# Performance work log

Hardware: AMD Instinct MI355X
Metric: run time of the kernel (lower is better)

## Reference

```python
import jax, jax.numpy as jnp
import numpy as np

S, N, L, D, H, V = 64, 128, 10, 300, 150, 50000


def setup_inputs() -> dict:
    key = jax.random.key(0)
    k0, k1, k2, k3 = jax.random.split(key, 4)
    tokens = jax.random.randint(k0, (S, N), 0, V)
    emb_table = jax.random.normal(k1, (V, D), jnp.float32) * 0.02
    W1 = jax.random.normal(k2, (D, H), jnp.float32) * (1.0 / np.sqrt(D))
    b1 = jnp.zeros((H,), jnp.float32)
    W2 = jax.random.normal(k3, (H, 1), jnp.float32) * (1.0 / np.sqrt(H))
    b2 = jnp.zeros((1,), jnp.float32)
    return {"tokens": tokens, "emb_table": emb_table, "W1": W1, "b1": b1, "W2": W2, "b2": b2}


def reference(tokens, emb_table, W1, b1, W2, b2):
    # word embeddings per sentence: [S, N, D]
    emb = emb_table[tokens]
    # FFNN attention score per token: Linear->ReLU->Linear(->1), squeeze -> [S, N]
    scores = (jax.nn.relu(emb @ W1 + b1) @ W2 + b2)[..., 0]

    n = tokens.shape[1]
    k = jnp.arange(L)                      # window position within span
    pos = jnp.arange(n)
    idx = pos[:, None] + k[None, :]        # [N, L] absolute token index of span (i, i+k)
    valid = idx < n                        # span position in-bounds
    idx_c = jnp.minimum(idx, n - 1)

    win_emb = emb[:, idx_c]                # [S, N, L, D]  emb[s, i+k]
    win_sc = scores[:, idx_c]              # [S, N, L]     scores[s, i+k]

    # tri[w, k] = (k <= w): positions belonging to span of width index w
    tri = k[:, None] >= k[None, :]                       # [L, L]
    m = tri[None, None] & valid[None, :, None, :]        # [1, N, L(w), L(k)]
    logits = jnp.where(m, win_sc[:, :, None, :], -jnp.inf)
    probs = jax.nn.softmax(logits, axis=-1)              # [S, N, Lw, Lk]
    head = jnp.einsum('snwk,snkd->snwd', probs, win_emb)  # softmax-weighted sum

    first = jnp.broadcast_to(emb[:, :, None, :], win_emb.shape)  # emb[i]
    last = win_emb                                               # emb[i+w] at k-axis == w
    out = jnp.concatenate([first, last, head], axis=-1)          # [S, N, L, 3D]
    # zero out spans that run past the sentence end
    return out * valid[None, :, :, None].astype(out.dtype)
```

## Files before the change

### kernel.cpp

```cpp
#include <hip/hip_runtime.h>
#include <cstddef>

#define SS 64
#define NN 128
#define LL 10
#define DD 300
#define HH 150
#define HP 152
#define CC 16
#define RMAX (CC + LL - 1)
#define JG 19
#define TG 13

#define WS_W1P 0
#define WS_BW  (DD*HP)

typedef float vf4 __attribute__((ext_vector_type(4)));

__device__ __forceinline__ void fma4(float4& a, float s, const float4 b) {
    a.x = fmaf(s, b.x, a.x);
    a.y = fmaf(s, b.y, a.y);
    a.z = fmaf(s, b.z, a.z);
    a.w = fmaf(s, b.w, a.w);
}

__device__ __forceinline__ void nt_store4(float* p, const float4 v) {
    vf4 t = {v.x, v.y, v.z, v.w};
    __builtin_nontemporal_store(t, (vf4*)p);
}

__global__ void pad_weights(const float* __restrict__ W1, const float* __restrict__ b1,
                            const float* __restrict__ W2, float* __restrict__ W1p,
                            float* __restrict__ bW) {
    int idx = blockIdx.x * 256 + threadIdx.x;
    if (idx < DD * HP) {
        int d = idx / HP, j = idx - d * HP;
        W1p[idx] = (j < HH) ? W1[d * HH + j] : 0.f;
    }
    if (idx < HP) {
        bW[idx] = (idx < HH) ? b1[idx] : 0.f;
    } else if (idx < 2 * HP) {
        int j = idx - HP;
        bW[idx] = (j < HH) ? W2[j] : 0.f;
    }
}

__global__ __launch_bounds__(256) void k_fused(
        const int* __restrict__ tokens, const float* __restrict__ table,
        const float* __restrict__ W1p, const float* __restrict__ bW,
        const float* __restrict__ b2, float* __restrict__ out)
{
    const int bid = blockIdx.x;
    const int s   = bid >> 3;
    const int i0  = (bid & 7) * CC;
    const int R   = min(RMAX, NN - i0);

    __shared__ float le[RMAX][DD + 4];
    __shared__ float lp[CC][LL][12];
    __shared__ float lpart[RMAX][20];
    __shared__ float sc_l[RMAX];
    __shared__ int   ltok[RMAX];

    const int tid = threadIdx.x;

    if (tid < R) ltok[tid] = tokens[s * NN + i0 + tid];
    __syncthreads();

    for (int l = tid; l < R * 75; l += 256) {
        const int t = l / 75, q = l - t * 75;
        *(float4*)&le[t][q * 4] = *(const float4*)(table + (size_t)ltok[t] * DD + q * 4);
    }
    __syncthreads();

    if (tid < TG * JG) {
        const int tg = tid / JG;
        const int jg = tid - tg * JG;
        const int t0 = tg * 2;
        if (t0 < R) {
            const int t1 = (t0 + 1 < R) ? (t0 + 1) : t0;
            const int j0 = jg * 8;
            const float* wp = W1p + j0;

            float4 a0l = {0,0,0,0}, a0h = {0,0,0,0}, a1l = {0,0,0,0}, a1h = {0,0,0,0};
            #pragma unroll 5
            for (int d = 0; d < DD; d += 4) {
                const float4 e0 = *(const float4*)&le[t0][d];
                const float4 e1 = *(const float4*)&le[t1][d];
                const float4 wa0 = *(const float4*)(wp + (size_t)(d + 0) * HP);
                const float4 wb0 = *(const float4*)(wp + (size_t)(d + 0) * HP + 4);
                const float4 wa1 = *(const float4*)(wp + (size_t)(d + 1) * HP);
                const float4 wb1 = *(const float4*)(wp + (size_t)(d + 1) * HP + 4);
                const float4 wa2 = *(const float4*)(wp + (size_t)(d + 2) * HP);
                const float4 wb2 = *(const float4*)(wp + (size_t)(d + 2) * HP + 4);
                const float4 wa3 = *(const float4*)(wp + (size_t)(d + 3) * HP);
                const float4 wb3 = *(const float4*)(wp + (size_t)(d + 3) * HP + 4);
                fma4(a0l, e0.x, wa0); fma4(a0h, e0.x, wb0);
                fma4(a0l, e0.y, wa1); fma4(a0h, e0.y, wb1);
                fma4(a0l, e0.z, wa2); fma4(a0h, e0.z, wb2);
                fma4(a0l, e0.w, wa3); fma4(a0h, e0.w, wb3);
                fma4(a1l, e1.x, wa0); fma4(a1h, e1.x, wb0);
                fma4(a1l, e1.y, wa1); fma4(a1h, e1.y, wb1);
                fma4(a1l, e1.z, wa2); fma4(a1h, e1.z, wb2);
                fma4(a1l, e1.w, wa3); fma4(a1h, e1.w, wb3);
            }
            const float4 bl = *(const float4*)(bW + j0);
            const float4 bh = *(const float4*)(bW + j0 + 4);
            const float4 vl = *(const float4*)(bW + HP + j0);
            const float4 vh = *(const float4*)(bW + HP + j0 + 4);

            #define RELD(A, B, V) (fmaxf((A).x + (B).x, 0.f) * (V).x + \
                                   fmaxf((A).y + (B).y, 0.f) * (V).y + \
                                   fmaxf((A).z + (B).z, 0.f) * (V).z + \
                                   fmaxf((A).w + (B).w, 0.f) * (V).w)
            lpart[t0][jg] = RELD(a0l, bl, vl) + RELD(a0h, bh, vh);
            if (t0 + 1 < R) lpart[t0 + 1][jg] = RELD(a1l, bl, vl) + RELD(a1h, bh, vh);
            #undef RELD
        }
    }
    __syncthreads();

    if (tid < R) {
        float sum = 0.f;
        #pragma unroll
        for (int jg = 0; jg < JG; ++jg) sum += lpart[tid][jg];
        sc_l[tid] = sum + b2[0];
    }
    __syncthreads();

    if (tid < CC * LL) {
        const int li = tid / LL, w = tid - li * LL;
        const int nk = min(LL, NN - (i0 + li));
        if (w < nk) {
            float m = -1e30f;
            for (int k = 0; k <= w; ++k) m = fmaxf(m, sc_l[li + k]);
            float sum = 0.f;
            for (int k = 0; k <= w; ++k) sum += __expf(sc_l[li + k] - m);
            const float inv = 1.f / sum;
            for (int k = 0; k <= w; ++k) lp[li][w][k] = __expf(sc_l[li + k] - m) * inv;
        }
    }
    __syncthreads();

    float* dst = out + (size_t)(s * NN + i0) * (LL * 3 * DD);
    for (int o4 = tid; o4 < CC * 2250; o4 += 256) {
        const int li = o4 / 2250;
        const int r  = o4 - li * 2250;
        const int w  = r / 225;
        const int c4 = r - w * 225;
        const int c  = c4 * 4;
        const int nk = min(LL, NN - (i0 + li));
        float4 v;
        if (w >= nk) {
            v = make_float4(0.f, 0.f, 0.f, 0.f);
        } else if (c < DD) {
            v = *(const float4*)&le[li][c];
        } else if (c < 2 * DD) {
            v = *(const float4*)&le[li + w][c - DD];
        } else {
            const int cc = c - 2 * DD;
            float4 a = make_float4(0.f, 0.f, 0.f, 0.f);
            for (int k = 0; k <= w; ++k) {
                fma4(a, lp[li][w][k], *(const float4*)&le[li + k][cc]);
            }
            v = a;
        }
        nt_store4(dst + (size_t)o4 * 4, v);
    }
}

extern "C" void kernel_launch(void* const* d_in, const int* in_sizes, int n_in,
                              void* d_out, int out_size, void* d_ws, size_t ws_size,
                              hipStream_t stream) {
    const int*   tokens = (const int*)d_in[0];
    const float* table  = (const float*)d_in[1];
    const float* W1     = (const float*)d_in[2];
    const float* b1     = (const float*)d_in[3];
    const float* W2     = (const float*)d_in[4];
    const float* b2     = (const float*)d_in[5];
    float* out = (float*)d_out;
    float* ws  = (float*)d_ws;

    float* W1p = ws + WS_W1P;
    float* bW  = ws + WS_BW;

    pad_weights<<<(DD * HP + 255) / 256, 256, 0, stream>>>(W1, b1, W2, W1p, bW);
    k_fused<<<SS * (NN / CC), 256, 0, stream>>>(tokens, table, W1p, bW, b2, out);
}
```

Measured before the change: 116.5 us.

## Halve per-block chunk, map output rows to waves, drop token staging

```diff
diff --git a/kernel.cpp b/kernel.cpp
--- a/kernel.cpp
+++ b/kernel.cpp
@@ -7,10 +7,10 @@
 #define DD 300
 #define HH 150
 #define HP 152
-#define CC 16
+#define CC 8
 #define RMAX (CC + LL - 1)
 #define JG 19
-#define TG 13
+#define TG 9
 
 #define WS_W1P 0
 #define WS_BW  (DD*HP)
@@ -45,30 +45,28 @@
     }
 }
 
-__global__ __launch_bounds__(256) void k_fused(
+__global__ __launch_bounds__(256, 4) void k_fused(
         const int* __restrict__ tokens, const float* __restrict__ table,
         const float* __restrict__ W1p, const float* __restrict__ bW,
         const float* __restrict__ b2, float* __restrict__ out)
 {
     const int bid = blockIdx.x;
-    const int s   = bid >> 3;
-    const int i0  = (bid & 7) * CC;
+    const int s   = bid >> 4;
+    const int i0  = (bid & 15) * CC;
     const int R   = min(RMAX, NN - i0);
 
     __shared__ float le[RMAX][DD + 4];
     __shared__ float lp[CC][LL][12];
     __shared__ float lpart[RMAX][20];
     __shared__ float sc_l[RMAX];
-    __shared__ int   ltok[RMAX];
 
     const int tid = threadIdx.x;
-
-    if (tid < R) ltok[tid] = tokens[s * NN + i0 + tid];
-    __syncthreads();
+    const int tokbase = s * NN + i0;
 
     for (int l = tid; l < R * 75; l += 256) {
         const int t = l / 75, q = l - t * 75;
-        *(float4*)&le[t][q * 4] = *(const float4*)(table + (size_t)ltok[t] * DD + q * 4);
+        const int tok = tokens[tokbase + t];
+        *(float4*)&le[t][q * 4] = *(const float4*)(table + (size_t)tok * DD + q * 4);
     }
     __syncthreads();
 
@@ -141,30 +139,34 @@
     }
     __syncthreads();
 
-    float* dst = out + (size_t)(s * NN + i0) * (LL * 3 * DD);
-    for (int o4 = tid; o4 < CC * 2250; o4 += 256) {
-        const int li = o4 / 2250;
-        const int r  = o4 - li * 2250;
-        const int w  = r / 225;
-        const int c4 = r - w * 225;
-        const int c  = c4 * 4;
+    const int wave = tid >> 6, lane = tid & 63;
+    float* dst = out + (size_t)tokbase * (LL * 3 * DD);
+    for (int pr = wave; pr < CC * LL; pr += 4) {
+        const int li = pr / LL, w = pr - li * LL;
         const int nk = min(LL, NN - (i0 + li));
-        float4 v;
-        if (w >= nk) {
-            v = make_float4(0.f, 0.f, 0.f, 0.f);
-        } else if (c < DD) {
-            v = *(const float4*)&le[li][c];
-        } else if (c < 2 * DD) {
-            v = *(const float4*)&le[li + w][c - DD];
-        } else {
-            const int cc = c - 2 * DD;
-            float4 a = make_float4(0.f, 0.f, 0.f, 0.f);
-            for (int k = 0; k <= w; ++k) {
-                fma4(a, lp[li][w][k], *(const float4*)&le[li + k][cc]);
+        const bool valid = (w < nk);
+        float* drow = dst + (size_t)pr * 900;
+        #pragma unroll
+        for (int rr = 0; rr < 4; ++rr) {
+            const int c4 = rr * 64 + lane;
+            if (c4 < 225) {
+                float4 v = make_float4(0.f, 0.f, 0.f, 0.f);
+                if (valid) {
+                    const int c = c4 * 4;
+                    if (c < DD) {
+                        v = *(const float4*)&le[li][c];
+                    } else if (c < 2 * DD) {
+                        v = *(const float4*)&le[li + w][c - DD];
+                    } else {
+                        const int cc = c - 2 * DD;
+                        for (int k = 0; k <= w; ++k) {
+                            fma4(v, lp[li][w][k], *(const float4*)&le[li + k][cc]);
+                        }
+                    }
+                }
+                nt_store4(drow + (size_t)c4 * 4, v);
             }
-            v = a;
         }
-        nt_store4(dst + (size_t)o4 * 4, v);
     }
 }
 
```

New measurement: 148.5 us. 1.27x slower.
